# Performance work log

Hardware: AMD Instinct MI355X
Metric: run time of the kernel (lower is better)

## Reference

```python
import jax, jax.numpy as jnp
import numpy as np

BSZ, SEQ, NVARS = 4, 512, 7
DM, NH, DFF, EL, FACTOR, PRED = 512, 8, 2048, 2, 5, 96
DH = DM // NH


def layer_norm(x, g, b, eps=1e-5):
    mu = jnp.mean(x, -1, keepdims=True)
    var = jnp.mean((x - mu) ** 2, -1, keepdims=True)
    return (x - mu) / jnp.sqrt(var + eps) * g + b


def prob_attention(q, k, v, key, factor=FACTOR):
    # q,k,v: (B,H,L,D); Informer ProbSparse self-attention (non-causal)
    B, H, L, D = q.shape
    Lk = k.shape[2]
    U_part = min(int(factor * np.ceil(np.log(Lk))), Lk)  # sampled keys per query
    u = min(int(factor * np.ceil(np.log(L))), L)         # top queries kept
    idx = jax.random.randint(key, (L, U_part), 0, Lk)
    k_s = k[:, :, idx]                                   # (B,H,L,U,D) gathered keys
    qk_s = jnp.einsum('bhld,bhlud->bhlu', q, k_s)
    M = qk_s.max(-1) - qk_s.sum(-1) / Lk                 # sparsity measure (div by L_K, as in Informer)
    _, top = jax.lax.top_k(M, u)                         # (B,H,u) active query indices
    q_r = jnp.take_along_axis(q, top[..., None], axis=2)  # (B,H,u,D)
    scale = np.float32(1.0 / np.sqrt(D))
    scores = jnp.einsum('bhud,bhkd->bhuk', q_r, k) * scale
    attn = jax.nn.softmax(scores, axis=-1)
    upd = jnp.einsum('bhuk,bhkd->bhud', attn, v)
    # initial context = mean of V for every query; overwrite active queries
    ctx = jnp.broadcast_to(jnp.mean(v, axis=2, keepdims=True), (B, H, L, D))
    bi = jnp.arange(B)[:, None, None]
    hi = jnp.arange(H)[None, :, None]
    return ctx.at[bi, hi, top].set(upd)


def encoder_layer(x, p, key):
    Wq, bq, Wk, bk, Wv, bv, Wo, bo, W1, b1, W2, b2, g1, be1, g2, be2 = p
    B, L, _ = x.shape
    q = (x @ Wq.T + bq).reshape(B, L, NH, DH).transpose(0, 2, 1, 3)
    k = (x @ Wk.T + bk).reshape(B, L, NH, DH).transpose(0, 2, 1, 3)
    v = (x @ Wv.T + bv).reshape(B, L, NH, DH).transpose(0, 2, 1, 3)
    ctx = prob_attention(q, k, v, key)
    out = ctx.transpose(0, 2, 1, 3).reshape(B, L, DM) @ Wo.T + bo
    x = layer_norm(x + out, g1, be1)
    y = jax.nn.gelu(x @ W1.T + b1) @ W2.T + b2
    return layer_norm(x + y, g2, be2)


def _forward(x_enc, w_emb, b_emb, w_pos, Wq, bq, Wk, bk, Wv, bv, Wo, bo,
             W1, b1, W2, b2, g1, be1, g2, be2, gF, bF, Wh, bh):
    B, L, V = x_enc.shape
    emb = x_enc[..., None] * w_emb + b_emb               # (B,L,V,DM)  Linear(1,DM) per scalar
    h = emb.transpose(0, 2, 1, 3).reshape(B * V, L, DM) + w_pos
    base = jax.random.key(42)
    for l in range(EL):
        p = (Wq[l], bq[l], Wk[l], bk[l], Wv[l], bv[l], Wo[l], bo[l],
             W1[l], b1[l], W2[l], b2[l], g1[l], be1[l], g2[l], be2[l])
        h = encoder_layer(h, p, jax.random.fold_in(base, l))
    h = layer_norm(h, gF, bF)
    h = h.reshape(B, V, L * DM)                          # flatten head: nf = SEQ*DM
    out = h @ Wh.T + bh                                  # (B,V,PRED)
    return out.transpose(0, 2, 1)                        # (B,PRED,V)


def setup_inputs() -> dict:
    key = jax.random.key(0)
    ks = jax.random.split(key, 32)
    s = 0.02
    d = {
        'x_enc': jax.random.normal(ks[0], (BSZ, SEQ, NVARS), jnp.float32),
        'w_emb': jax.random.normal(ks[1], (DM,), jnp.float32) * s,
        'b_emb': jnp.zeros((DM,), jnp.float32),
        'w_pos': jax.random.normal(ks[2], (SEQ, DM), jnp.float32) * s,
        'Wq': jax.random.normal(ks[3], (EL, DM, DM), jnp.float32) * s,
        'bq': jnp.zeros((EL, DM), jnp.float32),
        'Wk': jax.random.normal(ks[4], (EL, DM, DM), jnp.float32) * s,
        'bk': jnp.zeros((EL, DM), jnp.float32),
        'Wv': jax.random.normal(ks[5], (EL, DM, DM), jnp.float32) * s,
        'bv': jnp.zeros((EL, DM), jnp.float32),
        'Wo': jax.random.normal(ks[6], (EL, DM, DM), jnp.float32) * s,
        'bo': jnp.zeros((EL, DM), jnp.float32),
        'W1': jax.random.normal(ks[7], (EL, DFF, DM), jnp.float32) * s,
        'b1': jnp.zeros((EL, DFF), jnp.float32),
        'W2': jax.random.normal(ks[8], (EL, DM, DFF), jnp.float32) * s,
        'b2': jnp.zeros((EL, DM), jnp.float32),
        'g1': jnp.ones((EL, DM), jnp.float32),
        'be1': jnp.zeros((EL, DM), jnp.float32),
        'g2': jnp.ones((EL, DM), jnp.float32),
        'be2': jnp.zeros((EL, DM), jnp.float32),
        'gF': jnp.ones((DM,), jnp.float32),
        'bF': jnp.zeros((DM,), jnp.float32),
        'Wh': jax.random.normal(ks[9], (PRED, SEQ * DM), jnp.float32) * 0.002,
        'bh': jnp.zeros((PRED,), jnp.float32),
    }
    return d


def reference(x_enc, w_emb, b_emb, w_pos, Wq, bq, Wk, bk, Wv, bv, Wo, bo,
              W1, b1, W2, b2, g1, be1, g2, be2, gF, bF, Wh, bh):
    return _forward(x_enc, w_emb, b_emb, w_pos, Wq, bq, Wk, bk, Wv, bv, Wo, bo,
                    W1, b1, W2, b2, g1, be1, g2, be2, gF, bF, Wh, bh)
```

## Files before the change

kernel.cpp:

```cpp
#include <hip/hip_runtime.h>
#include <math.h>

#define SEQL 512
#define DMOD 512
#define NHEAD 8
#define DHEAD 64
#define DFFN 2048
#define NBATCH 4
#define NVARS 7
#define NBV 28
#define NBH 224
#define NROWS 14336
#define NSAMP 35
#define NPRED 96
#define SBIG 7340032
#define QKS 1024

typedef short bf16x8 __attribute__((ext_vector_type(8)));
typedef float f32x4 __attribute__((ext_vector_type(4)));

#define GLDS(gptr, lptr) \
  __builtin_amdgcn_global_load_lds((const __attribute__((address_space(1))) void*)(gptr), \
                                   (__attribute__((address_space(3))) void*)(lptr), 16, 0, 0)

__device__ inline unsigned short f2b(float f) {
  unsigned u = __builtin_bit_cast(unsigned, f);
  unsigned r = (u + 0x7FFFu + ((u >> 16) & 1u)) >> 16;
  return (unsigned short)r;
}
__device__ inline float b2f(unsigned short h) {
  return __builtin_bit_cast(float, (unsigned)h << 16);
}

__device__ inline void threefry2x32(unsigned k0, unsigned k1,
                                    unsigned x0, unsigned x1,
                                    unsigned &o0, unsigned &o1) {
  unsigned ks2 = k0 ^ k1 ^ 0x1BD11BDAu;
  unsigned ks[3] = {k0, k1, ks2};
  x0 += k0; x1 += k1;
  const unsigned rot[2][4] = {{13u,15u,26u,6u},{17u,29u,16u,24u}};
  #pragma unroll
  for (int i = 0; i < 5; ++i) {
    #pragma unroll
    for (int j = 0; j < 4; ++j) {
      unsigned r = rot[i & 1][j];
      x0 += x1;
      x1 = (x1 << r) | (x1 >> (32u - r));
      x1 ^= x0;
    }
    x0 += ks[(i + 1) % 3];
    x1 += ks[(i + 2) % 3] + (unsigned)(i + 1);
  }
  o0 = x0; o1 = x1;
}

__global__ void make_idx_kernel(int layer, int* idx) {
  int i = blockIdx.x * 256 + threadIdx.x;
  if (i >= SEQL * NSAMP) return;
  unsigned kl0, kl1, o0, o1;
  threefry2x32(0u, 42u, 0u, (unsigned)layer, kl0, kl1);
  threefry2x32(kl0, kl1, (unsigned)i, (unsigned)(SEQL * NSAMP + i), o0, o1);
  idx[i] = (int)(o1 & 511u);
}

__global__ void embed_kernel(const float* __restrict__ x_enc,
                             const float* __restrict__ w_emb,
                             const float* __restrict__ b_emb,
                             const float* __restrict__ w_pos,
                             float* __restrict__ h,
                             unsigned short* __restrict__ h_hi,
                             unsigned short* __restrict__ h_lo) {
  size_t i = (size_t)blockIdx.x * 256 + threadIdx.x;
  if (i >= (size_t)(SBIG / 4)) return;
  size_t e = i * 4;
  int dm = (int)(e & 511);
  int l  = (int)((e >> 9) & 511);
  int bv = (int)(e >> 18);
  int b = bv / NVARS, v = bv % NVARS;
  float xs = x_enc[((size_t)b * SEQL + l) * NVARS + v];
  float4 we = *(const float4*)(w_emb + dm);
  float4 bb = *(const float4*)(b_emb + dm);
  float4 wp = *(const float4*)(w_pos + (size_t)l * DMOD + dm);
  float4 val;
  val.x = xs * we.x + bb.x + wp.x;
  val.y = xs * we.y + bb.y + wp.y;
  val.z = xs * we.z + bb.z + wp.z;
  val.w = xs * we.w + bb.w + wp.w;
  *(float4*)(h + e) = val;
  ushort4 hi4, lo4;
  hi4.x = f2b(val.x); lo4.x = f2b(val.x - b2f(hi4.x));
  hi4.y = f2b(val.y); lo4.y = f2b(val.y - b2f(hi4.y));
  hi4.z = f2b(val.z); lo4.z = f2b(val.z - b2f(hi4.z));
  hi4.w = f2b(val.w); lo4.w = f2b(val.w - b2f(hi4.w));
  *(ushort4*)(h_hi + e) = hi4;
  *(ushort4*)(h_lo + e) = lo4;
}

__global__ void prep_weights(const float* __restrict__ Wq, const float* __restrict__ Wk,
                             const float* __restrict__ Wv, const float* __restrict__ Wo,
                             const float* __restrict__ W1, const float* __restrict__ W2,
                             unsigned short* __restrict__ Wqk_hi, unsigned short* __restrict__ Wqk_lo,
                             unsigned short* __restrict__ Wv_b, unsigned short* __restrict__ Wo_b,
                             unsigned short* __restrict__ W1_b, unsigned short* __restrict__ W2_b) {
  const int Q4 = 65536;
  int g = blockIdx.x * 256 + threadIdx.x;
  if (g < 2 * Q4) {
    const float* src = g < Q4 ? Wq : Wk;
    unsigned short* hi = Wqk_hi + (g < Q4 ? 0 : DMOD * DMOD);
    unsigned short* lo = Wqk_lo + (g < Q4 ? 0 : DMOD * DMOD);
    int off = (g < Q4 ? g : g - Q4) * 4;
    float4 v = *(const float4*)(src + off);
    ushort4 h4, l4;
    h4.x = f2b(v.x); l4.x = f2b(v.x - b2f(h4.x));
    h4.y = f2b(v.y); l4.y = f2b(v.y - b2f(h4.y));
    h4.z = f2b(v.z); l4.z = f2b(v.z - b2f(h4.z));
    h4.w = f2b(v.w); l4.w = f2b(v.w - b2f(h4.w));
    *(ushort4*)(hi + off) = h4;
    *(ushort4*)(lo + off) = l4;
    return;
  }
  const float* src;
  unsigned short* dst;
  int off;
  if (g < 3 * Q4)      { src = Wv; dst = Wv_b; off = (g - 2 * Q4) * 4; }
  else if (g < 4 * Q4) { src = Wo; dst = Wo_b; off = (g - 3 * Q4) * 4; }
  else if (g < 4 * Q4 + 262144) { src = W1; dst = W1_b; off = (g - 4 * Q4) * 4; }
  else                 { src = W2; dst = W2_b; off = (g - 4 * Q4 - 262144) * 4; }
  float4 v = *(const float4*)(src + off);
  ushort4 o;
  o.x = f2b(v.x); o.y = f2b(v.y); o.z = f2b(v.z); o.w = f2b(v.w);
  *(ushort4*)(dst + off) = o;
}

__global__ __launch_bounds__(256) void gemm_mfma3(const unsigned short* __restrict__ Ah,
                                                  const unsigned short* __restrict__ Al,
                                                  const unsigned short* __restrict__ Bh,
                                                  const unsigned short* __restrict__ Bl,
                                                  const float* __restrict__ bq,
                                                  const float* __restrict__ bk,
                                                  float* __restrict__ C,
                                                  int M, int N, int K, int ldc) {
  __shared__ __align__(16) unsigned short AsH[128 * 64];
  __shared__ __align__(16) unsigned short AsL[128 * 64];
  __shared__ __align__(16) unsigned short BsH[128 * 64];
  __shared__ __align__(16) unsigned short BsL[128 * 64];
  int nwg = gridDim.x * gridDim.y;
  int flat = blockIdx.y * gridDim.x + blockIdx.x;
  int swz = (flat & 7) * (nwg >> 3) + (flat >> 3);
  int bxs = swz % gridDim.x, bys = swz / gridDim.x;
  int bm = bys * 128, bn = bxs * 128;
  int tid = threadIdx.x;
  int wave = tid >> 6, lane = tid & 63;
  int wr = wave >> 1, wc = wave & 1;
  int r16 = lane & 15, kq = lane >> 4;

  f32x4 acc[4][4];
  #pragma unroll
  for (int i = 0; i < 4; ++i)
    #pragma unroll
    for (int j = 0; j < 4; ++j) acc[i][j] = (f32x4){0.f, 0.f, 0.f, 0.f};

  for (int kt = 0; kt < K; kt += 64) {
    __syncthreads();
    #pragma unroll
    for (int i = 0; i < 4; ++i) {
      int c = i * 256 + tid;
      int row = c >> 3, kb = c & 7;
      int kbs = kb ^ (row & 7);
      size_t offA = (size_t)(bm + row) * K + kt + kbs * 8;
      size_t offB = (size_t)(bn + row) * K + kt + kbs * 8;
      int ldst = (i * 256 + (tid & 192)) << 4;
      GLDS(Ah + offA, (char*)AsH + ldst);
      GLDS(Al + offA, (char*)AsL + ldst);
      GLDS(Bh + offB, (char*)BsH + ldst);
      GLDS(Bl + offB, (char*)BsL + ldst);
    }
    __syncthreads();
    #pragma unroll
    for (int ks = 0; ks < 2; ++ks) {
      bf16x8 ah[4], al[4], bh[4], bl[4];
      #pragma unroll
      for (int mi = 0; mi < 4; ++mi) {
        int row = wr * 64 + mi * 16 + r16;
        int addr = ((row << 7) | (ks << 6) | (kq << 4)) ^ ((row & 7) << 4);
        ah[mi] = *(const bf16x8*)((const char*)AsH + addr);
        al[mi] = *(const bf16x8*)((const char*)AsL + addr);
      }
      #pragma unroll
      for (int ni = 0; ni < 4; ++ni) {
        int row = wc * 64 + ni * 16 + r16;
        int addr = ((row << 7) | (ks << 6) | (kq << 4)) ^ ((row & 7) << 4);
        bh[ni] = *(const bf16x8*)((const char*)BsH + addr);
        bl[ni] = *(const bf16x8*)((const char*)BsL + addr);
      }
      #pragma unroll
      for (int mi = 0; mi < 4; ++mi)
        #pragma unroll
        for (int ni = 0; ni < 4; ++ni) {
          acc[mi][ni] = __builtin_amdgcn_mfma_f32_16x16x32_bf16(ah[mi], bh[ni], acc[mi][ni], 0, 0, 0);
          acc[mi][ni] = __builtin_amdgcn_mfma_f32_16x16x32_bf16(ah[mi], bl[ni], acc[mi][ni], 0, 0, 0);
          acc[mi][ni] = __builtin_amdgcn_mfma_f32_16x16x32_bf16(al[mi], bh[ni], acc[mi][ni], 0, 0, 0);
        }
    }
  }
  int crow0 = bm + wr * 64 + (lane >> 4) * 4;
  int ccol0 = bn + wc * 64 + (lane & 15);
  #pragma unroll
  for (int mi = 0; mi < 4; ++mi) {
    #pragma unroll
    for (int ni = 0; ni < 4; ++ni) {
      int col = ccol0 + ni * 16;
      float bvv = col < 512 ? bq[col] : bk[col - 512];
      #pragma unroll
      for (int r = 0; r < 4; ++r) {
        int row = crow0 + mi * 16 + r;
        C[(size_t)row * ldc + col] = acc[mi][ni][r] + bvv;
      }
    }
  }
}

template<int ACT, int OUTBF>
__global__ __launch_bounds__(256) void gemm_mfma(const unsigned short* __restrict__ A,
                                                 const unsigned short* __restrict__ W,
                                                 const float* __restrict__ bias,
                                                 float* __restrict__ Cf,
                                                 unsigned short* __restrict__ Cb,
                                                 int M, int N, int K) {
  __shared__ __align__(16) unsigned short As[2][128 * 64];
  __shared__ __align__(16) unsigned short Bs[2][128 * 64];
  int nwg = gridDim.x * gridDim.y;
  int flat = blockIdx.y * gridDim.x + blockIdx.x;
  int swz = (flat & 7) * (nwg >> 3) + (flat >> 3);
  int bxs = swz % gridDim.x, bys = swz / gridDim.x;
  int bm = bys * 128, bn = bxs * 128;
  int tid = threadIdx.x;
  int wave = tid >> 6, lane = tid & 63;
  int wr = wave >> 1, wc = wave & 1;
  int r16 = lane & 15, kq = lane >> 4;

  f32x4 acc[4][4];
  #pragma unroll
  for (int i = 0; i < 4; ++i)
    #pragma unroll
    for (int j = 0; j < 4; ++j) acc[i][j] = (f32x4){0.f, 0.f, 0.f, 0.f};

#define STAGE_MM(buf, ktv) \
  { \
    for (int i_ = 0; i_ < 4; ++i_) { \
      int c_ = i_ * 256 + tid; \
      int row_ = c_ >> 3, kb_ = c_ & 7; \
      int kbs_ = kb_ ^ (row_ & 7); \
      size_t offA_ = (size_t)(bm + row_) * K + (ktv) + kbs_ * 8; \
      size_t offB_ = (size_t)(bn + row_) * K + (ktv) + kbs_ * 8; \
      int ldst_ = (i_ * 256 + (tid & 192)) << 4; \
      GLDS(A + offA_, (char*)As[buf] + ldst_); \
      GLDS(W + offB_, (char*)Bs[buf] + ldst_); \
    } \
  }

  int nkt = K >> 6;
  STAGE_MM(0, 0);
  __syncthreads();
  for (int t = 0; t < nkt; ++t) {
    int cur = t & 1;
    if (t + 1 < nkt) STAGE_MM(cur ^ 1, (t + 1) << 6);
    const char* Ab = (const char*)As[cur];
    const char* Bb = (const char*)Bs[cur];
    #pragma unroll
    for (int ks = 0; ks < 2; ++ks) {
      bf16x8 afr[4], bfr[4];
      #pragma unroll
      for (int mi = 0; mi < 4; ++mi) {
        int row = wr * 64 + mi * 16 + r16;
        int addr = ((row << 7) | (ks << 6) | (kq << 4)) ^ ((row & 7) << 4);
        afr[mi] = *(const bf16x8*)(Ab + addr);
      }
      #pragma unroll
      for (int ni = 0; ni < 4; ++ni) {
        int row = wc * 64 + ni * 16 + r16;
        int addr = ((row << 7) | (ks << 6) | (kq << 4)) ^ ((row & 7) << 4);
        bfr[ni] = *(const bf16x8*)(Bb + addr);
      }
      #pragma unroll
      for (int mi = 0; mi < 4; ++mi)
        #pragma unroll
        for (int ni = 0; ni < 4; ++ni)
          acc[mi][ni] = __builtin_amdgcn_mfma_f32_16x16x32_bf16(afr[mi], bfr[ni], acc[mi][ni], 0, 0, 0);
    }
    __syncthreads();
  }
#undef STAGE_MM

  int crow0 = bm + wr * 64 + (lane >> 4) * 4;
  int ccol0 = bn + wc * 64 + (lane & 15);
  #pragma unroll
  for (int mi = 0; mi < 4; ++mi) {
    #pragma unroll
    for (int ni = 0; ni < 4; ++ni) {
      int col = ccol0 + ni * 16;
      float bvv = bias[col];
      #pragma unroll
      for (int r = 0; r < 4; ++r) {
        int row = crow0 + mi * 16 + r;
        float v = acc[mi][ni][r] + bvv;
        if (ACT) {
          float x = v;
          float u = x * __builtin_fmaf(0.044715f * x, x, 1.0f);
          float tme = __expf(-1.5957691216057308f * u);
          v = x * __builtin_amdgcn_rcpf(1.0f + tme);
        }
        if (OUTBF) Cb[(size_t)row * N + col] = f2b(v);
        else       Cf[(size_t)row * N + col] = v;
      }
    }
  }
}

__global__ __launch_bounds__(512) void m2_kernel(const float* __restrict__ QK,
                                                 const int* __restrict__ idx,
                                                 float* __restrict__ Mout) {
  int bh = blockIdx.x;
  int bv = bh >> 3, head = bh & 7;
  int tid = threadIdx.x;
  __shared__ float Ks[512 * 64];
  const float* base = QK + (size_t)bv * (SEQL * QKS);
  for (int c = tid; c < 512 * 16; c += 512) {
    int l = c >> 4, db = c & 15;
    float4 v = *(const float4*)(base + (size_t)l * QKS + 512 + head * 64 + db * 4);
    *(float4*)(Ks + l * 64 + ((db ^ (l & 15)) << 2)) = v;
  }
  float q[64];
  const float* qp = base + (size_t)tid * QKS + head * 64;
  #pragma unroll
  for (int d4 = 0; d4 < 64; d4 += 4) {
    float4 qv = *(const float4*)(qp + d4);
    q[d4 + 0] = qv.x; q[d4 + 1] = qv.y; q[d4 + 2] = qv.z; q[d4 + 3] = qv.w;
  }
  __syncthreads();
  const int* ip = idx + tid * NSAMP;
  float mx = -INFINITY, sm = 0.f;
  for (int u = 0; u < NSAMP; ++u) {
    int kidx = ip[u];
    const float* kr = Ks + kidx * 64;
    int x = kidx & 15;
    float s = 0.f;
    #pragma unroll
    for (int db = 0; db < 16; ++db) {
      float4 kv = *(const float4*)(kr + ((db ^ x) << 2));
      s += q[db * 4 + 0] * kv.x + q[db * 4 + 1] * kv.y
         + q[db * 4 + 2] * kv.z + q[db * 4 + 3] * kv.w;
    }
    mx = fmaxf(mx, s);
    sm += s;
  }
  Mout[(size_t)bh * SEQL + tid] = mx - sm * (1.0f / 512.0f);
}

__global__ __launch_bounds__(256) void topk_kernel(const float* __restrict__ Mv,
                                                   int* __restrict__ top) {
  int bh = blockIdx.x;
  int tid = threadIdx.x;
  __shared__ float vals[512];
  __shared__ float rv[256];
  __shared__ int ri[256];
  vals[tid]       = Mv[(size_t)bh * SEQL + tid];
  vals[tid + 256] = Mv[(size_t)bh * SEQL + tid + 256];
  __syncthreads();
  for (int t = 0; t < NSAMP; ++t) {
    float v0 = vals[tid], v1 = vals[tid + 256];
    float bvv; int bii;
    if (v0 >= v1) { bvv = v0; bii = tid; } else { bvv = v1; bii = tid + 256; }
    rv[tid] = bvv; ri[tid] = bii;
    __syncthreads();
    for (int s = 128; s > 0; s >>= 1) {
      if (tid < s) {
        float ov = rv[tid + s]; int oi = ri[tid + s];
        if (ov > rv[tid] || (ov == rv[tid] && oi < ri[tid])) { rv[tid] = ov; ri[tid] = oi; }
      }
      __syncthreads();
    }
    if (tid == 0) { top[bh * NSAMP + t] = ri[0]; vals[ri[0]] = -INFINITY; }
    __syncthreads();
  }
}

__global__ __launch_bounds__(256) void vmean_kernel(const unsigned short* __restrict__ Vb,
                                                    float* __restrict__ vmean) {
  int bv = blockIdx.x;
  int t = threadIdx.x;
  const unsigned short* vb = Vb + (size_t)bv * (SEQL * DMOD) + t * 2;
  float s0 = 0.f, s1 = 0.f;
  #pragma unroll 4
  for (int l = 0; l < SEQL; ++l) {
    unsigned u = *(const unsigned*)(vb + (size_t)l * DMOD);
    s0 += b2f((unsigned short)(u & 0xffffu));
    s1 += b2f((unsigned short)(u >> 16));
  }
  vmean[bv * DMOD + t * 2]     = s0 * (1.0f / 512.0f);
  vmean[bv * DMOD + t * 2 + 1] = s1 * (1.0f / 512.0f);
}

__global__ void ctx_fill_kernel(const float* __restrict__ vmean,
                                unsigned short* __restrict__ ctxb) {
  size_t i = (size_t)blockIdx.x * 256 + threadIdx.x;
  if (i >= (size_t)(SBIG / 4)) return;
  size_t e = i * 4;
  int dm = (int)(e & 511);
  int bv = (int)(e >> 18);
  float4 vm = *(const float4*)(vmean + bv * DMOD + dm);
  ushort4 o;
  o.x = f2b(vm.x); o.y = f2b(vm.y); o.z = f2b(vm.z); o.w = f2b(vm.w);
  *(ushort4*)(ctxb + e) = o;
}

__global__ __launch_bounds__(256) void attn2_kernel(const float* __restrict__ QK,
                                                    const unsigned short* __restrict__ Vb,
                                                    const int* __restrict__ top,
                                                    unsigned short* __restrict__ ctxb) {
  __shared__ __align__(16) unsigned short KV[512 * 64];
  __shared__ __align__(16) unsigned short P[48 * 512];
  __shared__ __align__(16) unsigned short Qs[48 * 64];
  __shared__ int topi[NSAMP];
  int bh = blockIdx.x;
  int bv = bh >> 3, head = bh & 7;
  int tid = threadIdx.x;
  int wv = tid >> 6, lane = tid & 63;
  int r16 = lane & 15, kq = lane >> 4;
  const float* base = QK + (size_t)bv * (SEQL * QKS);
  const unsigned short* vbase = Vb + (size_t)bv * (SEQL * DMOD) + head * 64;

  if (tid < NSAMP) topi[tid] = top[bh * NSAMP + tid];
  __syncthreads();

  for (int c = tid; c < NSAMP * 16; c += 256) {
    int u = c >> 4, dq = c & 15;
    float4 q4 = *(const float4*)(base + (size_t)topi[u] * QKS + head * 64 + dq * 4);
    ushort4 o;
    o.x = f2b(q4.x * 0.125f); o.y = f2b(q4.y * 0.125f);
    o.z = f2b(q4.z * 0.125f); o.w = f2b(q4.w * 0.125f);
    int byte = ((u << 7) | (dq << 3)) ^ ((u & 7) << 4);
    *(ushort4*)((char*)Qs + byte) = o;
  }
  for (int c = tid; c < 512 * 16; c += 256) {
    int l = c >> 4, dq = c & 15;
    float4 k4 = *(const float4*)(base + (size_t)l * QKS + 512 + head * 64 + dq * 4);
    ushort4 o;
    o.x = f2b(k4.x); o.y = f2b(k4.y); o.z = f2b(k4.z); o.w = f2b(k4.w);
    int byte = ((l << 7) | (dq << 3)) ^ ((l & 7) << 4);
    *(ushort4*)((char*)KV + byte) = o;
  }
  __syncthreads();

  {
    f32x4 acc[3][8];
    #pragma unroll
    for (int m = 0; m < 3; ++m)
      #pragma unroll
      for (int j = 0; j < 8; ++j) acc[m][j] = (f32x4){0.f, 0.f, 0.f, 0.f};
    bf16x8 afr[3][2];
    #pragma unroll
    for (int m = 0; m < 3; ++m)
      #pragma unroll
      for (int ks = 0; ks < 2; ++ks) {
        int row = m * 16 + r16;
        int addr = ((row << 7) | (ks << 6) | (kq << 4)) ^ ((row & 7) << 4);
        afr[m][ks] = *(const bf16x8*)((const char*)Qs + addr);
      }
    #pragma unroll
    for (int j = 0; j < 8; ++j) {
      int nrow = (wv * 8 + j) * 16 + r16;
      #pragma unroll
      for (int ks = 0; ks < 2; ++ks) {
        int addr = ((nrow << 7) | (ks << 6) | (kq << 4)) ^ ((nrow & 7) << 4);
        bf16x8 bfr = *(const bf16x8*)((const char*)KV + addr);
        #pragma unroll
        for (int m = 0; m < 3; ++m)
          acc[m][j] = __builtin_amdgcn_mfma_f32_16x16x32_bf16(afr[m][ks], bfr, acc[m][j], 0, 0, 0);
      }
    }
    #pragma unroll
    for (int m = 0; m < 3; ++m)
      #pragma unroll
      for (int j = 0; j < 8; ++j) {
        int l = (wv * 8 + j) * 16 + r16;
        #pragma unroll
        for (int r = 0; r < 4; ++r) {
          int u = m * 16 + kq * 4 + r;
          int byte = ((u << 10) | (l << 1)) ^ ((u & 7) << 4);
          *(unsigned short*)((char*)P + byte) = f2b(acc[m][j][r]);
        }
      }
  }
  __syncthreads();

  for (int c = tid; c < 512 * 8; c += 256) {
    int l = c >> 3, dq = c & 7;
    bf16x8 v8 = *(const bf16x8*)(vbase + (size_t)l * DMOD + dq * 8);
    #pragma unroll
    for (int j = 0; j < 8; ++j) {
      int d = dq * 8 + j;
      int byte = ((d << 10) | (l << 1)) ^ ((d & 7) << 4);
      *(unsigned short*)((char*)KV + byte) = (unsigned short)v8[j];
    }
  }
  for (int u = wv; u < NSAMP; u += 4) {
    int byte = ((u << 10) | (lane << 4)) ^ ((u & 7) << 4);
    bf16x8 sv = *(const bf16x8*)((const char*)P + byte);
    float s[8];
    #pragma unroll
    for (int j = 0; j < 8; ++j) s[j] = b2f((unsigned short)sv[j]);
    float mx = s[0];
    #pragma unroll
    for (int j = 1; j < 8; ++j) mx = fmaxf(mx, s[j]);
    #pragma unroll
    for (int off = 32; off > 0; off >>= 1) mx = fmaxf(mx, __shfl_xor(mx, off));
    float e[8], sm = 0.f;
    #pragma unroll
    for (int j = 0; j < 8; ++j) { e[j] = __expf(s[j] - mx); sm += e[j]; }
    #pragma unroll
    for (int off = 32; off > 0; off >>= 1) sm += __shfl_xor(sm, off);
    float inv = 1.0f / sm;
    bf16x8 pv;
    #pragma unroll
    for (int j = 0; j < 8; ++j) pv[j] = (short)f2b(e[j] * inv);
    *(bf16x8*)((char*)P + byte) = pv;
  }
  __syncthreads();

  {
    f32x4 acc2[3];
    #pragma unroll
    for (int m = 0; m < 3; ++m) acc2[m] = (f32x4){0.f, 0.f, 0.f, 0.f};
    for (int kst = 0; kst < 16; ++kst) {
      int vrow = wv * 16 + r16;
      int baddr = ((vrow << 10) | (kst << 6) | (kq << 4)) ^ ((vrow & 7) << 4);
      bf16x8 bfr = *(const bf16x8*)((const char*)KV + baddr);
      #pragma unroll
      for (int m = 0; m < 3; ++m) {
        int prow = m * 16 + r16;
        int aaddr = ((prow << 10) | (kst << 6) | (kq << 4)) ^ ((prow & 7) << 4);
        bf16x8 afr2 = *(const bf16x8*)((const char*)P + aaddr);
        acc2[m] = __builtin_amdgcn_mfma_f32_16x16x32_bf16(afr2, bfr, acc2[m], 0, 0, 0);
      }
    }
    int d = wv * 16 + r16;
    #pragma unroll
    for (int m = 0; m < 3; ++m)
      #pragma unroll
      for (int r = 0; r < 4; ++r) {
        int u = m * 16 + kq * 4 + r;
        if (u < NSAMP) {
          size_t off = (size_t)bv * (SEQL * DMOD) + (size_t)topi[u] * DMOD + head * 64 + d;
          ctxb[off] = f2b(acc2[m][r]);
        }
      }
  }
}

template<int BMODE, int OUT>
__global__ __launch_bounds__(256) void add_ln(const float* __restrict__ a,
                                              const unsigned short* __restrict__ b,
                                              const float* __restrict__ g,
                                              const float* __restrict__ be,
                                              float* __restrict__ out,
                                              unsigned short* __restrict__ outb,
                                              unsigned short* __restrict__ outh,
                                              unsigned short* __restrict__ outl) {
  int row = blockIdx.x * 2 + (threadIdx.x >> 7);
  int t = threadIdx.x & 127;
  int wave = threadIdx.x >> 6;
  int lane = threadIdx.x & 63;
  size_t base = (size_t)row * DMOD + t * 4;
  float4 x = *(const float4*)(a + base);
  if (BMODE == 2) {
    ushort4 r4 = *(const ushort4*)(b + base);
    x.x += b2f(r4.x); x.y += b2f(r4.y); x.z += b2f(r4.z); x.w += b2f(r4.w);
  }
  float s1 = x.x + x.y + x.z + x.w;
  float s2 = x.x * x.x + x.y * x.y + x.z * x.z + x.w * x.w;
  #pragma unroll
  for (int off = 32; off > 0; off >>= 1) {
    s1 += __shfl_xor(s1, off);
    s2 += __shfl_xor(s2, off);
  }
  __shared__ float sh[8];
  if (lane == 0) { sh[wave * 2] = s1; sh[wave * 2 + 1] = s2; }
  __syncthreads();
  int mate = wave ^ 1;
  s1 += sh[mate * 2];
  s2 += sh[mate * 2 + 1];
  float mu = s1 * (1.0f / 512.0f);
  float var = s2 * (1.0f / 512.0f) - mu * mu;
  float rstd = rsqrtf(var + 1e-5f);
  float4 gg = *(const float4*)(g + t * 4);
  float4 bb = *(const float4*)(be + t * 4);
  float4 o;
  o.x = (x.x - mu) * rstd * gg.x + bb.x;
  o.y = (x.y - mu) * rstd * gg.y + bb.y;
  o.z = (x.z - mu) * rstd * gg.z + bb.z;
  o.w = (x.w - mu) * rstd * gg.w + bb.w;
  *(float4*)(out + base) = o;
  if (OUT == 1) {
    ushort4 ob;
    ob.x = f2b(o.x); ob.y = f2b(o.y); ob.z = f2b(o.z); ob.w = f2b(o.w);
    *(ushort4*)(outb + base) = ob;
  }
  if (OUT == 2) {
    ushort4 hi4, lo4;
    hi4.x = f2b(o.x); lo4.x = f2b(o.x - b2f(hi4.x));
    hi4.y = f2b(o.y); lo4.y = f2b(o.y - b2f(hi4.y));
    hi4.z = f2b(o.z); lo4.z = f2b(o.z - b2f(hi4.z));
    hi4.w = f2b(o.w); lo4.w = f2b(o.w - b2f(hi4.w));
    *(ushort4*)(outh + base) = hi4;
    *(ushort4*)(outl + base) = lo4;
  }
}

__global__ __launch_bounds__(256) void head_partial_mfma(const unsigned short* __restrict__ hbf,
                                                         const float* __restrict__ Wh,
                                                         float* __restrict__ partial) {
  __shared__ __align__(16) unsigned short Hs[32 * 512];
  __shared__ __align__(16) unsigned short Ws[96 * 512];
  int blk = blockIdx.x;
  int k0 = blk * 512;
  int tid = threadIdx.x;
  int wv = tid >> 6, lane = tid & 63;
  int r16 = lane & 15, kq = lane >> 4;

  for (int c = tid; c < 32 * 64; c += 256) {
    int row = c >> 6, col8 = c & 63;
    int src = row < 28 ? row : 0;
    bf16x8 v = *(const bf16x8*)(hbf + (size_t)src * 262144 + k0 + col8 * 8);
    int byte = ((row << 10) | (col8 << 4)) ^ ((row & 7) << 4);
    *(bf16x8*)((char*)Hs + byte) = v;
  }
  for (int c = tid; c < 96 * 64; c += 256) {
    int row = c >> 6, col8 = c & 63;
    const float* src = Wh + (size_t)row * 262144 + k0 + col8 * 8;
    float4 va = *(const float4*)(src);
    float4 vb = *(const float4*)(src + 4);
    bf16x8 o8;
    o8[0] = (short)f2b(va.x); o8[1] = (short)f2b(va.y);
    o8[2] = (short)f2b(va.z); o8[3] = (short)f2b(va.w);
    o8[4] = (short)f2b(vb.x); o8[5] = (short)f2b(vb.y);
    o8[6] = (short)f2b(vb.z); o8[7] = (short)f2b(vb.w);
    int byte = ((row << 10) | (col8 << 4)) ^ ((row & 7) << 4);
    *(bf16x8*)((char*)Ws + byte) = o8;
  }
  __syncthreads();

  f32x4 acc[2][6];
  #pragma unroll
  for (int mt = 0; mt < 2; ++mt)
    #pragma unroll
    for (int nt = 0; nt < 6; ++nt) acc[mt][nt] = (f32x4){0.f, 0.f, 0.f, 0.f};

  #pragma unroll
  for (int kk = 0; kk < 4; ++kk) {
    int kfrag = wv * 4 + kk;
    bf16x8 afr[2];
    #pragma unroll
    for (int mt = 0; mt < 2; ++mt) {
      int row = mt * 16 + r16;
      int byte = ((row << 10) | (kfrag << 6) | (kq << 4)) ^ ((row & 7) << 4);
      afr[mt] = *(const bf16x8*)((const char*)Hs + byte);
    }
    #pragma unroll
    for (int nt = 0; nt < 6; ++nt) {
      int row = nt * 16 + r16;
      int byte = ((row << 10) | (kfrag << 6) | (kq << 4)) ^ ((row & 7) << 4);
      bf16x8 bfr = *(const bf16x8*)((const char*)Ws + byte);
      #pragma unroll
      for (int mt = 0; mt < 2; ++mt)
        acc[mt][nt] = __builtin_amdgcn_mfma_f32_16x16x32_bf16(afr[mt], bfr, acc[mt][nt], 0, 0, 0);
    }
  }
  size_t prow = (size_t)(blk * 4 + wv) * 2688;
  #pragma unroll
  for (int mt = 0; mt < 2; ++mt)
    #pragma unroll
    for (int nt = 0; nt < 6; ++nt)
      #pragma unroll
      for (int r = 0; r < 4; ++r) {
        int m = mt * 16 + kq * 4 + r;
        int n = nt * 16 + r16;
        if (m < 28) partial[prow + m * 96 + n] = acc[mt][nt][r];
      }
}

__global__ __launch_bounds__(256) void head_reduce(const float* __restrict__ partial,
                                                   const float* __restrict__ bh_,
                                                   float* __restrict__ out) {
  int o = blockIdx.x;
  int tid = threadIdx.x;
  float s = 0.f;
  for (int b = tid; b < 2048; b += 256) s += partial[(size_t)b * 2688 + o];
  __shared__ float red[256];
  red[tid] = s;
  __syncthreads();
  for (int st = 128; st > 0; st >>= 1) {
    if (tid < st) red[tid] += red[tid + st];
    __syncthreads();
  }
  if (tid == 0) {
    int m = o / 96, p = o % 96;
    int b = m / NVARS, v = m % NVARS;
    out[(size_t)b * (NPRED * NVARS) + (size_t)p * NVARS + v] = red[0] + bh_[p];
  }
}

extern "C" void kernel_launch(void* const* d_in, const int* in_sizes, int n_in,
                              void* d_out, int out_size, void* d_ws, size_t ws_size,
                              hipStream_t stream) {
  const float* x_enc = (const float*)d_in[0];
  const float* w_emb = (const float*)d_in[1];
  const float* b_emb = (const float*)d_in[2];
  const float* w_pos = (const float*)d_in[3];
  const float* Wq = (const float*)d_in[4];
  const float* bq = (const float*)d_in[5];
  const float* Wk = (const float*)d_in[6];
  const float* bk = (const float*)d_in[7];
  const float* Wv = (const float*)d_in[8];
  const float* bv_ = (const float*)d_in[9];
  const float* Wo = (const float*)d_in[10];
  const float* bo = (const float*)d_in[11];
  const float* W1 = (const float*)d_in[12];
  const float* b1 = (const float*)d_in[13];
  const float* W2 = (const float*)d_in[14];
  const float* b2 = (const float*)d_in[15];
  const float* g1 = (const float*)d_in[16];
  const float* be1 = (const float*)d_in[17];
  const float* g2 = (const float*)d_in[18];
  const float* be2 = (const float*)d_in[19];
  const float* gF = (const float*)d_in[20];
  const float* bF = (const float*)d_in[21];
  const float* Wh = (const float*)d_in[22];
  const float* bh_ = (const float*)d_in[23];
  float* out = (float*)d_out;

  const size_t S = (size_t)SBIG;
  const size_t SB = S * 4;
  char* ws = (char*)d_ws;
  float* h    = (float*)(ws);
  float* QKb  = (float*)(ws + SB);
  unsigned short* Vb   = (unsigned short*)(ws + 3 * SB);
  unsigned short* Ob_b = (unsigned short*)(ws + 3 * SB + SB / 2);
  unsigned short* Wqk_hi = (unsigned short*)(ws + 4 * SB);
  unsigned short* Wqk_lo = (unsigned short*)(ws + 4 * SB + 0x100000);
  unsigned short* Wv_b = (unsigned short*)(ws + 4 * SB + 0x200000);
  unsigned short* Wo_b = (unsigned short*)(ws + 4 * SB + 0x280000);
  unsigned short* W1_b = (unsigned short*)(ws + 4 * SB + 0x300000);
  unsigned short* W2_b = (unsigned short*)(ws + 4 * SB + 0x500000);
  unsigned short* h_hi = (unsigned short*)(ws + 5 * SB);
  unsigned short* h_lo = (unsigned short*)(ws + 5 * SB + SB / 2);
  unsigned short* CTXb = h_hi;
  unsigned short* h_bf = h_lo;
  unsigned short* FFNb = (unsigned short*)QKb;
  float* partial = QKb;
  int*   idx = (int*)(ws + 6 * SB);
  float* Mv  = (float*)(ws + 6 * SB + 0x20000);
  int*   top = (int*)(ws + 6 * SB + 0xA0000);
  float* vmean = (float*)(ws + 6 * SB + 0xB0000);
  if (ws_size < 6 * SB + 0xC0000) return;

  dim3 b256(256);
  int gVec = (int)(S / 4 / 256);

  embed_kernel<<<gVec, b256, 0, stream>>>(x_enc, w_emb, b_emb, w_pos, h, h_hi, h_lo);

  for (int l = 0; l < 2; ++l) {
    const float* Wql = Wq + (size_t)l * DMOD * DMOD;
    const float* Wkl = Wk + (size_t)l * DMOD * DMOD;
    const float* Wvl = Wv + (size_t)l * DMOD * DMOD;
    const float* Wol = Wo + (size_t)l * DMOD * DMOD;
    const float* W1l = W1 + (size_t)l * DFFN * DMOD;
    const float* W2l = W2 + (size_t)l * DMOD * DFFN;

    prep_weights<<<3072, b256, 0, stream>>>(Wql, Wkl, Wvl, Wol, W1l, W2l,
                                            Wqk_hi, Wqk_lo, Wv_b, Wo_b, W1_b, W2_b);

    dim3 gqk(QKS / 128, NROWS / 128);
    gemm_mfma3<<<gqk, b256, 0, stream>>>(h_hi, h_lo, Wqk_hi, Wqk_lo,
                                         bq + l * DMOD, bk + l * DMOD,
                                         QKb, NROWS, QKS, DMOD, QKS);
    dim3 gv(DMOD / 128, NROWS / 128);
    gemm_mfma<0, 1><<<gv, b256, 0, stream>>>(h_hi, Wv_b, bv_ + l * DMOD,
                                             (float*)0, Vb, NROWS, DMOD, DMOD);

    make_idx_kernel<<<(SEQL * NSAMP + 255) / 256, b256, 0, stream>>>(l, idx);
    m2_kernel<<<NBH, dim3(512), 0, stream>>>(QKb, idx, Mv);
    topk_kernel<<<NBH, b256, 0, stream>>>(Mv, top);
    vmean_kernel<<<NBV, b256, 0, stream>>>(Vb, vmean);
    ctx_fill_kernel<<<gVec, b256, 0, stream>>>(vmean, CTXb);
    attn2_kernel<<<NBH, b256, 0, stream>>>(QKb, Vb, top, CTXb);

    dim3 go(DMOD / 128, NROWS / 128);
    gemm_mfma<0, 1><<<go, b256, 0, stream>>>(CTXb, Wo_b, bo + l * DMOD,
                                             (float*)0, Ob_b, NROWS, DMOD, DMOD);
    add_ln<2, 1><<<NROWS / 2, b256, 0, stream>>>(h, Ob_b, g1 + l * DMOD, be1 + l * DMOD,
                                                 h, h_bf, (unsigned short*)0, (unsigned short*)0);

    dim3 gf1(DFFN / 128, NROWS / 128);
    gemm_mfma<1, 1><<<gf1, b256, 0, stream>>>(h_bf, W1_b, b1 + l * DFFN,
                                              (float*)0, FFNb, NROWS, DFFN, DMOD);
    dim3 gf2(DMOD / 128, NROWS / 128);
    gemm_mfma<0, 1><<<gf2, b256, 0, stream>>>(FFNb, W2_b, b2 + l * DMOD,
                                              (float*)0, Ob_b, NROWS, DMOD, DFFN);
    if (l == 0) {
      add_ln<2, 2><<<NROWS / 2, b256, 0, stream>>>(h, Ob_b, g2 + l * DMOD, be2 + l * DMOD,
                                                   h, (unsigned short*)0, h_hi, h_lo);
    } else {
      add_ln<2, 0><<<NROWS / 2, b256, 0, stream>>>(h, Ob_b, g2 + l * DMOD, be2 + l * DMOD,
                                                   h, (unsigned short*)0, (unsigned short*)0, (unsigned short*)0);
    }
  }

  add_ln<0, 1><<<NROWS / 2, b256, 0, stream>>>(h, (const unsigned short*)0, gF, bF,
                                               h, h_bf, (unsigned short*)0, (unsigned short*)0);
  head_partial_mfma<<<512, b256, 0, stream>>>(h_bf, Wh, partial);
  head_reduce<<<NBV * NPRED, b256, 0, stream>>>(partial, bh_, out);
}
```

Baseline: 754.3 us.

## Fuse sparsity scoring with top-k, split V-mean reduction, coalesce head reduce

Merges the sparsity-measure kernel and the top-k selection into one kernel that reuses the shared K buffer for the reduction, so the M values never round-trip through global memory and one launch is saved. The V-mean is now computed by 8x more blocks over 64-row slices, and ctx_fill sums the partial results, which spreads a previously 28-block reduction across more CUs. The head reduction now has each block handle 32 outputs with coalesced reads instead of one output per block with strided reads. The top-k reduction now uses a 512-wide tree with one extra level per iteration.

```diff
diff --git a/kernel.cpp b/kernel.cpp
--- a/kernel.cpp
+++ b/kernel.cpp
@@ -317,9 +317,9 @@
   }
 }
 
-__global__ __launch_bounds__(512) void m2_kernel(const float* __restrict__ QK,
-                                                 const int* __restrict__ idx,
-                                                 float* __restrict__ Mout) {
+__global__ __launch_bounds__(512) void m2_topk_kernel(const float* __restrict__ QK,
+                                                      const int* __restrict__ idx,
+                                                      int* __restrict__ top) {
   int bh = blockIdx.x;
   int bv = bh >> 3, head = bh & 7;
   int tid = threadIdx.x;
@@ -354,26 +354,18 @@
     mx = fmaxf(mx, s);
     sm += s;
   }
-  Mout[(size_t)bh * SEQL + tid] = mx - sm * (1.0f / 512.0f);
-}
-
-__global__ __launch_bounds__(256) void topk_kernel(const float* __restrict__ Mv,
-                                                   int* __restrict__ top) {
-  int bh = blockIdx.x;
-  int tid = threadIdx.x;
-  __shared__ float vals[512];
-  __shared__ float rv[256];
-  __shared__ int ri[256];
-  vals[tid]       = Mv[(size_t)bh * SEQL + tid];
-  vals[tid + 256] = Mv[(size_t)bh * SEQL + tid + 256];
+  float Mval = mx - sm * (1.0f / 512.0f);
+  __syncthreads();
+  float* vals = Ks;
+  float* rv   = Ks + 512;
+  int*   ri   = (int*)(Ks + 1024);
+  vals[tid] = Mval;
   __syncthreads();
   for (int t = 0; t < NSAMP; ++t) {
-    float v0 = vals[tid], v1 = vals[tid + 256];
-    float bvv; int bii;
-    if (v0 >= v1) { bvv = v0; bii = tid; } else { bvv = v1; bii = tid + 256; }
-    rv[tid] = bvv; ri[tid] = bii;
+    rv[tid] = vals[tid];
+    ri[tid] = tid;
     __syncthreads();
-    for (int s = 128; s > 0; s >>= 1) {
+    for (int s = 256; s > 0; s >>= 1) {
       if (tid < s) {
         float ov = rv[tid + s]; int oi = ri[tid + s];
         if (ov > rv[tid] || (ov == rv[tid] && oi < ri[tid])) { rv[tid] = ov; ri[tid] = oi; }
@@ -385,32 +377,40 @@
   }
 }
 
-__global__ __launch_bounds__(256) void vmean_kernel(const unsigned short* __restrict__ Vb,
-                                                    float* __restrict__ vmean) {
-  int bv = blockIdx.x;
+__global__ __launch_bounds__(256) void vmean_part_kernel(const unsigned short* __restrict__ Vb,
+                                                         float* __restrict__ part) {
+  int blk = blockIdx.x;
+  int bv = blk >> 3, grp = blk & 7;
   int t = threadIdx.x;
-  const unsigned short* vb = Vb + (size_t)bv * (SEQL * DMOD) + t * 2;
+  const unsigned short* vb = Vb + (size_t)bv * (SEQL * DMOD) + (size_t)grp * 64 * DMOD + t * 2;
   float s0 = 0.f, s1 = 0.f;
   #pragma unroll 4
-  for (int l = 0; l < SEQL; ++l) {
+  for (int l = 0; l < 64; ++l) {
     unsigned u = *(const unsigned*)(vb + (size_t)l * DMOD);
     s0 += b2f((unsigned short)(u & 0xffffu));
     s1 += b2f((unsigned short)(u >> 16));
   }
-  vmean[bv * DMOD + t * 2]     = s0 * (1.0f / 512.0f);
-  vmean[bv * DMOD + t * 2 + 1] = s1 * (1.0f / 512.0f);
-}
-
-__global__ void ctx_fill_kernel(const float* __restrict__ vmean,
+  part[(size_t)blk * DMOD + t * 2]     = s0;
+  part[(size_t)blk * DMOD + t * 2 + 1] = s1;
+}
+
+__global__ void ctx_fill_kernel(const float* __restrict__ part,
                                 unsigned short* __restrict__ ctxb) {
   size_t i = (size_t)blockIdx.x * 256 + threadIdx.x;
   if (i >= (size_t)(SBIG / 4)) return;
   size_t e = i * 4;
   int dm = (int)(e & 511);
   int bv = (int)(e >> 18);
-  float4 vm = *(const float4*)(vmean + bv * DMOD + dm);
+  float4 vm = {0.f, 0.f, 0.f, 0.f};
+  #pragma unroll
+  for (int g = 0; g < 8; ++g) {
+    float4 p = *(const float4*)(part + (size_t)(bv * 8 + g) * DMOD + dm);
+    vm.x += p.x; vm.y += p.y; vm.z += p.z; vm.w += p.w;
+  }
+  const float inv = 1.0f / 512.0f;
   ushort4 o;
-  o.x = f2b(vm.x); o.y = f2b(vm.y); o.z = f2b(vm.z); o.w = f2b(vm.w);
+  o.x = f2b(vm.x * inv); o.y = f2b(vm.y * inv);
+  o.z = f2b(vm.z * inv); o.w = f2b(vm.w * inv);
   *(ushort4*)(ctxb + e) = o;
 }
 
@@ -692,21 +692,24 @@
 __global__ __launch_bounds__(256) void head_reduce(const float* __restrict__ partial,
                                                    const float* __restrict__ bh_,
                                                    float* __restrict__ out) {
-  int o = blockIdx.x;
-  int tid = threadIdx.x;
+  int blk = blockIdx.x;
+  int o0 = blk * 32;
+  int oo = threadIdx.x & 31;
+  int rp = threadIdx.x >> 5;
   float s = 0.f;
-  for (int b = tid; b < 2048; b += 256) s += partial[(size_t)b * 2688 + o];
+  for (int r = rp; r < 2048; r += 8)
+    s += partial[(size_t)r * 2688 + o0 + oo];
   __shared__ float red[256];
-  red[tid] = s;
-  __syncthreads();
-  for (int st = 128; st > 0; st >>= 1) {
-    if (tid < st) red[tid] += red[tid + st];
-    __syncthreads();
-  }
-  if (tid == 0) {
+  red[threadIdx.x] = s;
+  __syncthreads();
+  if (rp == 0) {
+    float tot = 0.f;
+    #pragma unroll
+    for (int k = 0; k < 8; ++k) tot += red[k * 32 + oo];
+    int o = o0 + oo;
     int m = o / 96, p = o % 96;
     int b = m / NVARS, v = m % NVARS;
-    out[(size_t)b * (NPRED * NVARS) + (size_t)p * NVARS + v] = red[0] + bh_[p];
+    out[(size_t)b * (NPRED * NVARS) + (size_t)p * NVARS + v] = tot + bh_[p];
   }
 }
 
@@ -759,9 +762,8 @@
   unsigned short* FFNb = (unsigned short*)QKb;
   float* partial = QKb;
   int*   idx = (int*)(ws + 6 * SB);
-  float* Mv  = (float*)(ws + 6 * SB + 0x20000);
+  float* vpart = (float*)(ws + 6 * SB + 0x20000);
   int*   top = (int*)(ws + 6 * SB + 0xA0000);
-  float* vmean = (float*)(ws + 6 * SB + 0xB0000);
   if (ws_size < 6 * SB + 0xC0000) return;
 
   dim3 b256(256);
@@ -789,10 +791,9 @@
                                              (float*)0, Vb, NROWS, DMOD, DMOD);
 
     make_idx_kernel<<<(SEQL * NSAMP + 255) / 256, b256, 0, stream>>>(l, idx);
-    m2_kernel<<<NBH, dim3(512), 0, stream>>>(QKb, idx, Mv);
-    topk_kernel<<<NBH, b256, 0, stream>>>(Mv, top);
-    vmean_kernel<<<NBV, b256, 0, stream>>>(Vb, vmean);
-    ctx_fill_kernel<<<gVec, b256, 0, stream>>>(vmean, CTXb);
+    m2_topk_kernel<<<NBH, dim3(512), 0, stream>>>(QKb, idx, top);
+    vmean_part_kernel<<<NBV * 8, b256, 0, stream>>>(Vb, vpart);
+    ctx_fill_kernel<<<gVec, b256, 0, stream>>>(vpart, CTXb);
     attn2_kernel<<<NBH, b256, 0, stream>>>(QKb, Vb, top, CTXb);
 
     dim3 go(DMOD / 128, NROWS / 128);
@@ -819,5 +820,5 @@
   add_ln<0, 1><<<NROWS / 2, b256, 0, stream>>>(h, (const unsigned short*)0, gF, bF,
                                                h, h_bf, (unsigned short*)0, (unsigned short*)0);
   head_partial_mfma<<<512, b256, 0, stream>>>(h_bf, Wh, partial);
-  head_reduce<<<NBV * NPRED, b256, 0, stream>>>(partial, bh_, out);
-}
+  head_reduce<<<84, b256, 0, stream>>>(partial, bh_, out);
+}
```

Measured after the change: 752.5 us. Within noise of the previous version (-0.2%).
